# Performance work log

Hardware: AMD Instinct MI355X
Metric: run time of the kernel (lower is better)

The kernel has to match this reference:

```python
import jax, jax.numpy as jnp
import numpy as np

B, N, C, H = 2, 2048, 512, 8
D = C // H
SCALE = D ** (-0.5)


def setup_inputs() -> dict:
    key = jax.random.key(0)
    k1, k2, k3 = jax.random.split(key, 3)
    x = jax.random.normal(k1, (B, N, C), dtype=jnp.float32)
    qkv_w = jax.random.normal(k2, (C, 3 * C), dtype=jnp.float32) * (C ** -0.5)
    proj_w = jax.random.normal(k3, (C, C), dtype=jnp.float32) * (C ** -0.5)
    proj_b = jnp.zeros((C,), dtype=jnp.float32)
    return {"x": x, "qkv_w": qkv_w, "proj_w": proj_w, "proj_b": proj_b}


def reference(x, qkv_w, proj_w, proj_b):
    # qkv projection (no bias) -> (B, N, 3, H, D) -> (3, B, H, N, D)
    qkv = jnp.einsum('bnc,cf->bnf', x, qkv_w)
    qkv = qkv.reshape(B, N, 3, H, D).transpose(2, 0, 3, 1, 4)
    q, k, v = qkv[0], qkv[1], qkv[2]
    q = q * SCALE
    attn = jnp.einsum('bhid,bhjd->bhij', q, k)          # (B, H, N, N)
    attn = jax.nn.softmax(attn, axis=-1)
    out = jnp.einsum('bhij,bhjd->bhid', attn, v)         # (B, H, N, D)
    # Faithful to source: reshape (B,H,N,D) -> (B,N,C) WITHOUT transposing
    out = out.reshape(B, N, C)
    out = jnp.einsum('bnc,cd->bnd', out, proj_w) + proj_b
    return out
```

## Files before the change

### kernel.cpp

```cpp
#include <hip/hip_runtime.h>
#include <math.h>

constexpr int Bb = 2;
constexpr int Nn = 2048;
constexpr int Cc = 512;
constexpr int Hh = 8;
constexpr int Dd = 64;

typedef short short8 __attribute__((ext_vector_type(8)));
typedef float floatx4 __attribute__((ext_vector_type(4)));
typedef float floatx16 __attribute__((ext_vector_type(16)));

__device__ inline short8 bcs8(uint4 u) { return __builtin_bit_cast(short8, u); }

__device__ inline floatx4 mfma16(short8 a, short8 b, floatx4 c) {
    return __builtin_amdgcn_mfma_f32_16x16x32_bf16(a, b, c, 0, 0, 0);
}
__device__ inline floatx16 mfma32(short8 a, short8 b, floatx16 c) {
    return __builtin_amdgcn_mfma_f32_32x32x16_bf16(a, b, c, 0, 0, 0);
}

typedef __attribute__((address_space(1))) void gvoid;
typedef __attribute__((address_space(3))) void svoid;
__device__ inline void glds16(const void* g, void* l) {
    __builtin_amdgcn_global_load_lds((const gvoid*)g, (svoid*)l, 16, 0, 0);
}

#if __has_builtin(__builtin_amdgcn_exp2f)
#define EXP2(x) __builtin_amdgcn_exp2f(x)
#else
#define EXP2(x) __expf((x) * 0.69314718056f)
#endif

__device__ inline unsigned pk_trunc(float a, float b) {
    return __builtin_amdgcn_perm(__float_as_uint(b), __float_as_uint(a), 0x07060302u);
}
__device__ inline unsigned pk_rne(float a, float b) {
    unsigned ua = __float_as_uint(a); ua += 0x7fffu + ((ua >> 16) & 1u);
    unsigned ub = __float_as_uint(b); ub += 0x7fffu + ((ub >> 16) & 1u);
    return __builtin_amdgcn_perm(ub, ua, 0x07060302u);
}
__device__ inline unsigned short rne1(float a) {
    unsigned u = __float_as_uint(a); u += 0x7fffu + ((u >> 16) & 1u);
    return (unsigned short)(u >> 16);
}
__device__ inline float tr16(float a) {
    return __uint_as_float(__float_as_uint(a) & 0xffff0000u);
}
__device__ inline void split8(float4 A, float4 B, uint4& hi, uint4& lo) {
    hi = make_uint4(pk_trunc(A.x, A.y), pk_trunc(A.z, A.w),
                    pk_trunc(B.x, B.y), pk_trunc(B.z, B.w));
    lo = make_uint4(pk_trunc(A.x - tr16(A.x), A.y - tr16(A.y)),
                    pk_trunc(A.z - tr16(A.z), A.w - tr16(A.w)),
                    pk_trunc(B.x - tr16(B.x), B.y - tr16(B.y)),
                    pk_trunc(B.z - tr16(B.z), B.w - tr16(B.w)));
}

__global__ __launch_bounds__(256) void prep(const float* __restrict__ qkv_w,
                                            const float* __restrict__ proj_w,
                                            const float* __restrict__ x,
                                            unsigned short* __restrict__ wqh,
                                            unsigned short* __restrict__ wql,
                                            unsigned short* __restrict__ wph,
                                            unsigned short* __restrict__ wpl,
                                            unsigned short* __restrict__ xh,
                                            unsigned short* __restrict__ xl)
{
    __shared__ float Tl[64][68];
    int bid = blockIdx.x;
    if (bid >= 256) {
        size_t base = ((size_t)(bid - 256) * 256 + threadIdx.x) * 16;
        float4 a = *(const float4*)(x + base);
        float4 b = *(const float4*)(x + base + 4);
        float4 c = *(const float4*)(x + base + 8);
        float4 d = *(const float4*)(x + base + 12);
        uint4 h0, L0, h1, L1;
        split8(a, b, h0, L0); split8(c, d, h1, L1);
        *(uint4*)(xh + base) = h0; *(uint4*)(xh + base + 8) = h1;
        *(uint4*)(xl + base) = L0; *(uint4*)(xl + base + 8) = L1;
        return;
    }
    const float* src; unsigned short *dh, *dlo; int W, f0, k0;
    if (bid < 192) { int kt = bid / 24, ft = bid % 24; W = 1536; src = qkv_w; dh = wqh; dlo = wql; f0 = ft * 64; k0 = kt * 64; }
    else { int b2 = bid - 192; int kt = b2 / 8, ft = b2 % 8; W = 512; src = proj_w; dh = wph; dlo = wpl; f0 = ft * 64; k0 = kt * 64; }
    int t = threadIdx.x;
    {
        int kl = t >> 2, fc = (t & 3) * 16;
        const float* p = src + (size_t)(k0 + kl) * W + f0 + fc;
        #pragma unroll
        for (int i = 0; i < 4; ++i) {
            float4 v = *(const float4*)(p + i * 4);
            Tl[kl][fc + i * 4 + 0] = v.x; Tl[kl][fc + i * 4 + 1] = v.y;
            Tl[kl][fc + i * 4 + 2] = v.z; Tl[kl][fc + i * 4 + 3] = v.w;
        }
    }
    __syncthreads();
    {
        int fl = t >> 2, kc = (t & 3) * 16;
        float v[16];
        #pragma unroll
        for (int i = 0; i < 16; ++i) v[i] = Tl[kc + i][fl];
        unsigned hi[8], lo[8];
        #pragma unroll
        for (int i = 0; i < 8; ++i) {
            float a = v[2 * i], b = v[2 * i + 1];
            hi[i] = pk_trunc(a, b);
            lo[i] = pk_trunc(a - tr16(a), b - tr16(b));
        }
        unsigned short* oh = dh + (size_t)(f0 + fl) * 512 + k0 + kc;
        unsigned short* ol = dlo + (size_t)(f0 + fl) * 512 + k0 + kc;
        *(uint4*)oh = make_uint4(hi[0], hi[1], hi[2], hi[3]);
        *(uint4*)(oh + 8) = make_uint4(hi[4], hi[5], hi[6], hi[7]);
        *(uint4*)ol = make_uint4(lo[0], lo[1], lo[2], lo[3]);
        *(uint4*)(ol + 8) = make_uint4(lo[4], lo[5], lo[6], lo[7]);
    }
}

__global__ __launch_bounds__(256, 3) void gemm_qkv(const unsigned short* __restrict__ xh,
                                                   const unsigned short* __restrict__ xl,
                                                   const unsigned short* __restrict__ wh,
                                                   const unsigned short* __restrict__ wl,
                                                   unsigned short* __restrict__ qd,
                                                   unsigned short* __restrict__ kd,
                                                   unsigned short* __restrict__ vt)
{
    __shared__ __align__(16) char smem[49152];
    const int tid = threadIdx.x, lane = tid & 63, w = tid >> 6;
    const int l15 = lane & 15, l4 = lane >> 4;
    const int row0 = blockIdx.y * 128, col0 = blockIdx.x * 64;
    const int wm = w >> 1, wn = w & 1;

    floatx4 acc[4][2];
    #pragma unroll
    for (int i = 0; i < 4; ++i)
        #pragma unroll
        for (int j = 0; j < 2; ++j)
            #pragma unroll
            for (int r = 0; r < 4; ++r) acc[i][j][r] = 0.f;

    auto stage = [&](int k0, char* buf) {
        char* Ah = buf; char* Al = buf + 8192; char* Bh = buf + 16384; char* Bl = buf + 20480;
        #pragma unroll
        for (int i = 0; i < 4; ++i) {
            int sid = w * 4 + i; int mt = sid >> 1, comp = sid & 1;
            const unsigned short* src = (comp ? xl : xh) + (size_t)(row0 + mt * 16 + l15) * 512 + k0 + l4 * 8;
            glds16(src, (comp ? Al : Ah) + mt * 1024);
        }
        #pragma unroll
        for (int i = 0; i < 2; ++i) {
            int sid = w * 2 + i; int nt = sid >> 1, comp = sid & 1;
            const unsigned short* src = (comp ? wl : wh) + (size_t)(col0 + nt * 16 + l15) * 512 + k0 + l4 * 8;
            glds16(src, (comp ? Bl : Bh) + nt * 1024);
        }
    };

    stage(0, smem);
    for (int it = 0; it < 16; ++it) {
        __syncthreads();
        char* buf = smem + (it & 1) * 24576;
        if (it < 15) stage((it + 1) * 32, smem + ((it + 1) & 1) * 24576);
        char* Ah = buf; char* Al = buf + 8192; char* Bh = buf + 16384; char* Bl = buf + 20480;
        short8 af[4][2], bf[2][2];
        #pragma unroll
        for (int mt = 0; mt < 4; ++mt) {
            int off = ((wm * 4 + mt) << 10) + (lane << 4);
            af[mt][0] = bcs8(*(const uint4*)(Ah + off));
            af[mt][1] = bcs8(*(const uint4*)(Al + off));
        }
        #pragma unroll
        for (int nt = 0; nt < 2; ++nt) {
            int off = ((wn * 2 + nt) << 10) + (lane << 4);
            bf[nt][0] = bcs8(*(const uint4*)(Bh + off));
            bf[nt][1] = bcs8(*(const uint4*)(Bl + off));
        }
        #pragma unroll
        for (int mt = 0; mt < 4; ++mt)
            #pragma unroll
            for (int nt = 0; nt < 2; ++nt) {
                acc[mt][nt] = mfma16(af[mt][0], bf[nt][0], acc[mt][nt]);
                acc[mt][nt] = mfma16(af[mt][0], bf[nt][1], acc[mt][nt]);
                acc[mt][nt] = mfma16(af[mt][1], bf[nt][0], acc[mt][nt]);
            }
    }
    #pragma unroll
    for (int mt = 0; mt < 4; ++mt)
        #pragma unroll
        for (int nt = 0; nt < 2; ++nt) {
            int c = col0 + (wn * 2 + nt) * 16 + l15;
            int which = c >> 9;
            int head = (c >> 6) & 7, d = c & 63;
            int tokb = row0 + (wm * 4 + mt) * 16 + l4 * 4;
            int b = tokb >> 11, n = tokb & 2047;
            if (which == 2) {
                uint2 pv;
                pv.x = pk_rne(acc[mt][nt][0], acc[mt][nt][1]);
                pv.y = pk_rne(acc[mt][nt][2], acc[mt][nt][3]);
                *(uint2*)&vt[((size_t)((b * 8 + head) * 64 + d)) * 2048 + n] = pv;
            } else {
                unsigned short* dst = which ? kd : qd;
                float s = which ? 1.0f : 0.18033688f;
                #pragma unroll
                for (int r = 0; r < 4; ++r)
                    dst[(size_t)((b * 8 + head) * 2048 + n + r) * 64 + d] = rne1(acc[mt][nt][r] * s);
            }
        }
}

__global__ __launch_bounds__(512, 4) void attn(const unsigned short* __restrict__ qd,
                                               const unsigned short* __restrict__ kd,
                                               const unsigned short* __restrict__ vt,
                                               unsigned short* __restrict__ Oh,
                                               unsigned short* __restrict__ Ol)
{
    __shared__ __align__(16) char smem[65536];

    int bid = blockIdx.x;
    int xcd = bid & 7; int rr = bid >> 3;
    int qt = rr & 31; int bhi = rr >> 5;
    int bh = (bhi << 3) | xcd;
    int tid = threadIdx.x, lane = tid & 63, w = tid >> 6;
    int qg = w >> 2, kg = w & 3;
    int l31 = lane & 31, h = lane >> 5;

    short8 qf[4];
    #pragma unroll
    for (int s = 0; s < 4; ++s)
        qf[s] = bcs8(*(const uint4*)(qd + ((size_t)bh * 2048 + qt * 64 + qg * 32 + l31) * 64 + s * 16 + h * 8));

    const uint4 onesu = make_uint4(0x3F803F80u, 0x3F803F80u, 0x3F803F80u, 0x3F803F80u);
    const short8 onesf = bcs8(onesu);

    floatx16 OT[2], OTl;
    #pragma unroll
    for (int i = 0; i < 2; ++i)
        #pragma unroll
        for (int r = 0; r < 16; ++r) OT[i][r] = 0.f;
    #pragma unroll
    for (int r = 0; r < 16; ++r) OTl[r] = 0.f;

    auto stage = [&](int c, char* buf) {
        int ks0 = c * 128;
        #pragma unroll
        for (int i = 0; i < 4; ++i) {
            int sid = w * 4 + i;
            if (sid < 16) {
                int mt = sid >> 2, s = sid & 3;
                const unsigned short* src = kd + (size_t)(bh * 2048 + ks0 + mt * 32 + l31) * 64 + s * 16 + h * 8;
                glds16(src, buf + sid * 1024);
            } else {
                int s2 = sid - 16; int mtv = s2 >> 3, sv = s2 & 7;
                const unsigned short* src = vt + (size_t)(bh * 64 + mtv * 32 + l31) * 2048 + ks0 + sv * 16 + h * 8;
                glds16(src, buf + 16384 + s2 * 1024);
            }
        }
    };

    stage(0, smem);
    for (int c = 0; c < 16; ++c) {
        __syncthreads();
        char* cbuf = smem + (c & 1) * 32768;
        if (c < 15) stage(c + 1, smem + ((c + 1) & 1) * 32768);

        char* Kst = cbuf; char* Vst = cbuf + 16384;
        short8 kf[4];
        #pragma unroll
        for (int s = 0; s < 4; ++s)
            kf[s] = bcs8(*(const uint4*)(Kst + ((kg << 2) + s) * 1024 + (lane << 4)));
        short8 vf[2][2];
        #pragma unroll
        for (int kc = 0; kc < 2; ++kc) {
            int sv = kg * 2 + kc;
            vf[kc][0] = bcs8(*(const uint4*)(Vst + sv * 1024 + (lane << 4)));
            vf[kc][1] = bcs8(*(const uint4*)(Vst + (8 + sv) * 1024 + (lane << 4)));
        }

        floatx16 st;
        #pragma unroll
        for (int r = 0; r < 16; ++r) st[r] = 0.f;
        #pragma unroll
        for (int s = 0; s < 4; ++s) st = mfma32(kf[s], qf[s], st);

        unsigned P2[8];
        #pragma unroll
        for (int s2 = 0; s2 < 8; ++s2)
            P2[s2] = pk_trunc(EXP2(st[2 * s2]), EXP2(st[2 * s2 + 1]));

        #pragma unroll
        for (int kc = 0; kc < 2; ++kc) {
            unsigned X0 = P2[4 * kc + 0], X1 = P2[4 * kc + 1];
            unsigned Y0 = P2[4 * kc + 2], Y1 = P2[4 * kc + 3];
            unsigned Xo0 = __shfl_xor(X0, 32, 64), Xo1 = __shfl_xor(X1, 32, 64);
            unsigned Yo0 = __shfl_xor(Y0, 32, 64), Yo1 = __shfl_xor(Y1, 32, 64);
            uint4 fu;
            fu.x = h ? Yo0 : X0;
            fu.y = h ? Yo1 : X1;
            fu.z = h ? Y0 : Xo0;
            fu.w = h ? Y1 : Xo1;
            short8 pf = bcs8(fu);
            OT[0] = mfma32(vf[kc][0], pf, OT[0]);
            OT[1] = mfma32(vf[kc][1], pf, OT[1]);
            OTl = mfma32(onesf, pf, OTl);
        }
    }

    float* Mq = (float*)smem + qg * 2048;
    float* Lq = (float*)(smem + 32768) + qg * 64;
    float* Tq = (float*)(smem + 32768 + 512) + qg * 2176;

    __syncthreads();
    if (kg == 3) {
        #pragma unroll
        for (int mtv = 0; mtv < 2; ++mtv)
            #pragma unroll
            for (int r = 0; r < 16; ++r) {
                int d = mtv * 32 + (r & 3) + 8 * (r >> 2) + 4 * h;
                Mq[d * 32 + l31] = OT[mtv][r];
            }
        Lq[h * 32 + l31] = OTl[0];
    }
    __syncthreads();
    if (kg == 2) {
        #pragma unroll
        for (int mtv = 0; mtv < 2; ++mtv)
            #pragma unroll
            for (int r = 0; r < 16; ++r) {
                int d = mtv * 32 + (r & 3) + 8 * (r >> 2) + 4 * h;
                Mq[d * 32 + l31] += OT[mtv][r];
            }
        Lq[h * 32 + l31] += OTl[0];
    }
    __syncthreads();
    if (kg == 1) {
        #pragma unroll
        for (int mtv = 0; mtv < 2; ++mtv)
            #pragma unroll
            for (int r = 0; r < 16; ++r) {
                int d = mtv * 32 + (r & 3) + 8 * (r >> 2) + 4 * h;
                Mq[d * 32 + l31] += OT[mtv][r];
            }
        Lq[h * 32 + l31] += OTl[0];
    }
    __syncthreads();
    if (kg == 0) {
        #pragma unroll
        for (int mtv = 0; mtv < 2; ++mtv)
            #pragma unroll
            for (int r = 0; r < 16; ++r) {
                int d = mtv * 32 + (r & 3) + 8 * (r >> 2) + 4 * h;
                OT[mtv][r] += Mq[d * 32 + l31];
            }
        float inv = 1.f / (Lq[h * 32 + l31] + OTl[0]);
        #pragma unroll
        for (int mtv = 0; mtv < 2; ++mtv)
            #pragma unroll
            for (int r = 0; r < 16; ++r) {
                int d = mtv * 32 + (r & 3) + 8 * (r >> 2) + 4 * h;
                Tq[l31 * 68 + d] = OT[mtv][r] * inv;
            }
    }
    __syncthreads();
    {
        int q = tid >> 3, dc = (tid & 7) * 8;
        const float* T = (const float*)(smem + 32768 + 512) + (q >> 5) * 2176;
        int ql = q & 31;
        float vv[8];
        #pragma unroll
        for (int i = 0; i < 8; ++i) vv[i] = T[ql * 68 + dc + i];
        unsigned hi[4], lo[4];
        #pragma unroll
        for (int i = 0; i < 4; ++i) {
            float a = vv[2 * i], bb = vv[2 * i + 1];
            hi[i] = pk_trunc(a, bb);
            lo[i] = pk_trunc(a - tr16(a), bb - tr16(bb));
        }
        size_t bo = ((size_t)(bh * 2048 + qt * 64 + q)) * 64 + dc;
        *(uint4*)(Oh + bo) = make_uint4(hi[0], hi[1], hi[2], hi[3]);
        *(uint4*)(Ol + bo) = make_uint4(lo[0], lo[1], lo[2], lo[3]);
    }
}

__global__ __launch_bounds__(256, 2) void gemm_proj(const unsigned short* __restrict__ Ah_g,
                                                    const unsigned short* __restrict__ Al_g,
                                                    const unsigned short* __restrict__ wh,
                                                    const unsigned short* __restrict__ wl,
                                                    const float* __restrict__ bias,
                                                    float* __restrict__ out)
{
    __shared__ __align__(16) char smem[32768];
    const int tid = threadIdx.x, lane = tid & 63, w = tid >> 6;
    const int l15 = lane & 15, l4 = lane >> 4;
    const int row0 = blockIdx.y * 64, col0 = blockIdx.x * 64;
    const int wm = w >> 1, wn = w & 1;

    floatx4 acc[2][2];
    #pragma unroll
    for (int i = 0; i < 2; ++i)
        #pragma unroll
        for (int j = 0; j < 2; ++j)
            #pragma unroll
            for (int r = 0; r < 4; ++r) acc[i][j][r] = 0.f;

    auto stage = [&](int k0, char* buf) {
        #pragma unroll
        for (int i = 0; i < 4; ++i) {
            int sid = w * 4 + i;
            if (sid < 8) {
                int mt = sid >> 1, comp = sid & 1;
                const unsigned short* src = (comp ? Al_g : Ah_g) + (size_t)(row0 + mt * 16 + l15) * 512 + k0 + l4 * 8;
                glds16(src, buf + (comp ? 4096 : 0) + mt * 1024);
            } else {
                int s2 = sid - 8; int nt = s2 >> 1, comp = s2 & 1;
                const unsigned short* src = (comp ? wl : wh) + (size_t)(col0 + nt * 16 + l15) * 512 + k0 + l4 * 8;
                glds16(src, buf + (comp ? 12288 : 8192) + nt * 1024);
            }
        }
    };

    stage(0, smem);
    for (int it = 0; it < 16; ++it) {
        __syncthreads();
        char* buf = smem + (it & 1) * 16384;
        if (it < 15) stage((it + 1) * 32, smem + ((it + 1) & 1) * 16384);
        char* Ah = buf; char* Al = buf + 4096; char* Bh = buf + 8192; char* Bl = buf + 12288;
        short8 af[2][2], bf[2][2];
        #pragma unroll
        for (int mt = 0; mt < 2; ++mt) {
            int off = ((wm * 2 + mt) << 10) + (lane << 4);
            af[mt][0] = bcs8(*(const uint4*)(Ah + off));
            af[mt][1] = bcs8(*(const uint4*)(Al + off));
        }
        #pragma unroll
        for (int nt = 0; nt < 2; ++nt) {
            int off = ((wn * 2 + nt) << 10) + (lane << 4);
            bf[nt][0] = bcs8(*(const uint4*)(Bh + off));
            bf[nt][1] = bcs8(*(const uint4*)(Bl + off));
        }
        #pragma unroll
        for (int mt = 0; mt < 2; ++mt)
            #pragma unroll
            for (int nt = 0; nt < 2; ++nt) {
                acc[mt][nt] = mfma16(af[mt][0], bf[nt][0], acc[mt][nt]);
                acc[mt][nt] = mfma16(af[mt][0], bf[nt][1], acc[mt][nt]);
                acc[mt][nt] = mfma16(af[mt][1], bf[nt][0], acc[mt][nt]);
            }
    }
    #pragma unroll
    for (int mt = 0; mt < 2; ++mt)
        #pragma unroll
        for (int nt = 0; nt < 2; ++nt) {
            int c = col0 + (wn * 2 + nt) * 16 + l15;
            float bv = bias[c];
            #pragma unroll
            for (int r = 0; r < 4; ++r) {
                int tok = row0 + (wm * 2 + mt) * 16 + l4 * 4 + r;
                out[(size_t)tok * 512 + c] = acc[mt][nt][r] + bv;
            }
        }
}

extern "C" void kernel_launch(void* const* d_in, const int* in_sizes, int n_in,
                              void* d_out, int out_size, void* d_ws, size_t ws_size,
                              hipStream_t stream)
{
    const float* x      = (const float*)d_in[0];
    const float* qkv_w  = (const float*)d_in[1];
    const float* proj_w = (const float*)d_in[2];
    const float* proj_b = (const float*)d_in[3];
    float* out = (float*)d_out;

    char* ws = (char*)d_ws;
    unsigned short* qd   = (unsigned short*)ws;
    unsigned short* kd   = (unsigned short*)(ws + 4194304);
    unsigned short* vt   = (unsigned short*)(ws + 8388608);
    unsigned short* wqh  = (unsigned short*)(ws + 12582912);
    unsigned short* wql  = (unsigned short*)(ws + 14155776);
    unsigned short* wph  = (unsigned short*)(ws + 15728640);
    unsigned short* wpl  = (unsigned short*)(ws + 16252928);
    unsigned short* Oh   = (unsigned short*)(ws + 16777216);
    unsigned short* Ol   = (unsigned short*)(ws + 20971520);
    unsigned short* xh = Oh;
    unsigned short* xl = Ol;

    prep<<<768, 256, 0, stream>>>(qkv_w, proj_w, x, wqh, wql, wph, wpl, xh, xl);
    gemm_qkv<<<dim3(24, 32), 256, 0, stream>>>(xh, xl, wqh, wql, qd, kd, vt);
    attn<<<512, 512, 0, stream>>>(qd, kd, vt, Oh, Ol);
    gemm_proj<<<dim3(8, 64), 256, 0, stream>>>(Oh, Ol, wph, wpl, proj_b, out);
}
```

Baseline: 165.7 us.

## Fuse x bf16 split into QKV GEMM, load K to registers in attention

Removes the x hi/lo split pass from the prep kernel. The QKV GEMM now stages raw fp32 x tiles into LDS and splits them into bf16 hi/lo in registers just before the MFMAs, which avoids writing and re-reading two bf16 copies of x. In the attention kernel, K fragments are loaded straight from global memory into double-buffered registers instead of going through LDS, and LDS now stages only V, so shared memory shrinks. The P-fragment shuffle also drops from four cross-half shuffles to two per step, at the cost of more VGPRs and redundant per-block split arithmetic.

After: 173.2 us. 4.5% more time.

```diff
diff --git a/kernel.cpp b/kernel.cpp
--- a/kernel.cpp
+++ b/kernel.cpp
@@ -12,6 +12,7 @@
 typedef float floatx16 __attribute__((ext_vector_type(16)));
 
 __device__ inline short8 bcs8(uint4 u) { return __builtin_bit_cast(short8, u); }
+__device__ inline float4 bcf4(uint4 u) { return __builtin_bit_cast(float4, u); }
 
 __device__ inline floatx4 mfma16(short8 a, short8 b, floatx4 c) {
     return __builtin_amdgcn_mfma_f32_16x16x32_bf16(a, b, c, 0, 0, 0);
@@ -58,28 +59,13 @@
 
 __global__ __launch_bounds__(256) void prep(const float* __restrict__ qkv_w,
                                             const float* __restrict__ proj_w,
-                                            const float* __restrict__ x,
                                             unsigned short* __restrict__ wqh,
                                             unsigned short* __restrict__ wql,
                                             unsigned short* __restrict__ wph,
-                                            unsigned short* __restrict__ wpl,
-                                            unsigned short* __restrict__ xh,
-                                            unsigned short* __restrict__ xl)
+                                            unsigned short* __restrict__ wpl)
 {
     __shared__ float Tl[64][68];
     int bid = blockIdx.x;
-    if (bid >= 256) {
-        size_t base = ((size_t)(bid - 256) * 256 + threadIdx.x) * 16;
-        float4 a = *(const float4*)(x + base);
-        float4 b = *(const float4*)(x + base + 4);
-        float4 c = *(const float4*)(x + base + 8);
-        float4 d = *(const float4*)(x + base + 12);
-        uint4 h0, L0, h1, L1;
-        split8(a, b, h0, L0); split8(c, d, h1, L1);
-        *(uint4*)(xh + base) = h0; *(uint4*)(xh + base + 8) = h1;
-        *(uint4*)(xl + base) = L0; *(uint4*)(xl + base + 8) = L1;
-        return;
-    }
     const float* src; unsigned short *dh, *dlo; int W, f0, k0;
     if (bid < 192) { int kt = bid / 24, ft = bid % 24; W = 1536; src = qkv_w; dh = wqh; dlo = wql; f0 = ft * 64; k0 = kt * 64; }
     else { int b2 = bid - 192; int kt = b2 / 8, ft = b2 % 8; W = 512; src = proj_w; dh = wph; dlo = wpl; f0 = ft * 64; k0 = kt * 64; }
@@ -116,8 +102,7 @@
     }
 }
 
-__global__ __launch_bounds__(256, 3) void gemm_qkv(const unsigned short* __restrict__ xh,
-                                                   const unsigned short* __restrict__ xl,
+__global__ __launch_bounds__(256, 3) void gemm_qkv(const float* __restrict__ x,
                                                    const unsigned short* __restrict__ wh,
                                                    const unsigned short* __restrict__ wl,
                                                    unsigned short* __restrict__ qd,
@@ -139,18 +124,17 @@
             for (int r = 0; r < 4; ++r) acc[i][j][r] = 0.f;
 
     auto stage = [&](int k0, char* buf) {
-        char* Ah = buf; char* Al = buf + 8192; char* Bh = buf + 16384; char* Bl = buf + 20480;
         #pragma unroll
         for (int i = 0; i < 4; ++i) {
-            int sid = w * 4 + i; int mt = sid >> 1, comp = sid & 1;
-            const unsigned short* src = (comp ? xl : xh) + (size_t)(row0 + mt * 16 + l15) * 512 + k0 + l4 * 8;
-            glds16(src, (comp ? Al : Ah) + mt * 1024);
+            int sid = w * 4 + i; int mt = sid >> 1, sub = sid & 1;
+            const float* src = x + (size_t)(row0 + mt * 16 + l15) * 512 + k0 + l4 * 8 + sub * 4;
+            glds16(src, buf + sid * 1024);
         }
         #pragma unroll
         for (int i = 0; i < 2; ++i) {
             int sid = w * 2 + i; int nt = sid >> 1, comp = sid & 1;
             const unsigned short* src = (comp ? wl : wh) + (size_t)(col0 + nt * 16 + l15) * 512 + k0 + l4 * 8;
-            glds16(src, (comp ? Bl : Bh) + nt * 1024);
+            glds16(src, buf + 16384 + comp * 4096 + nt * 1024);
         }
     };
 
@@ -159,13 +143,17 @@
         __syncthreads();
         char* buf = smem + (it & 1) * 24576;
         if (it < 15) stage((it + 1) * 32, smem + ((it + 1) & 1) * 24576);
-        char* Ah = buf; char* Al = buf + 8192; char* Bh = buf + 16384; char* Bl = buf + 20480;
+        char* Ab = buf; char* Bh = buf + 16384; char* Bl = buf + 20480;
         short8 af[4][2], bf[2][2];
         #pragma unroll
         for (int mt = 0; mt < 4; ++mt) {
-            int off = ((wm * 4 + mt) << 10) + (lane << 4);
-            af[mt][0] = bcs8(*(const uint4*)(Ah + off));
-            af[mt][1] = bcs8(*(const uint4*)(Al + off));
+            int off = (((wm * 4 + mt) * 2) << 10) + (lane << 4);
+            float4 fa = bcf4(*(const uint4*)(Ab + off));
+            float4 fb = bcf4(*(const uint4*)(Ab + off + 1024));
+            uint4 hi, lo;
+            split8(fa, fb, hi, lo);
+            af[mt][0] = bcs8(hi);
+            af[mt][1] = bcs8(lo);
         }
         #pragma unroll
         for (int nt = 0; nt < 2; ++nt) {
@@ -212,7 +200,7 @@
                                                unsigned short* __restrict__ Oh,
                                                unsigned short* __restrict__ Ol)
 {
-    __shared__ __align__(16) char smem[65536];
+    __shared__ __align__(16) char smem[51200];
 
     int bid = blockIdx.x;
     int xcd = bid & 7; int rr = bid >> 3;
@@ -238,34 +226,34 @@
     #pragma unroll
     for (int r = 0; r < 16; ++r) OTl[r] = 0.f;
 
-    auto stage = [&](int c, char* buf) {
+    auto stageV = [&](int c, char* buf) {
         int ks0 = c * 128;
         #pragma unroll
-        for (int i = 0; i < 4; ++i) {
-            int sid = w * 4 + i;
-            if (sid < 16) {
-                int mt = sid >> 2, s = sid & 3;
-                const unsigned short* src = kd + (size_t)(bh * 2048 + ks0 + mt * 32 + l31) * 64 + s * 16 + h * 8;
-                glds16(src, buf + sid * 1024);
-            } else {
-                int s2 = sid - 16; int mtv = s2 >> 3, sv = s2 & 7;
-                const unsigned short* src = vt + (size_t)(bh * 64 + mtv * 32 + l31) * 2048 + ks0 + sv * 16 + h * 8;
-                glds16(src, buf + 16384 + s2 * 1024);
-            }
+        for (int i = 0; i < 2; ++i) {
+            int sid = w * 2 + i; int mtv = sid >> 3, sv = sid & 7;
+            const unsigned short* src = vt + (size_t)(bh * 64 + mtv * 32 + l31) * 2048 + ks0 + sv * 16 + h * 8;
+            glds16(src, buf + sid * 1024);
         }
     };
 
-    stage(0, smem);
+    const unsigned short* kb_ = kd + ((size_t)bh * 2048 + kg * 32 + l31) * 64 + h * 8;
+    uint4 kfb[2][4];
+    #pragma unroll
+    for (int s = 0; s < 4; ++s) kfb[0][s] = *(const uint4*)(kb_ + s * 16);
+    stageV(0, smem);
+
+    #pragma unroll
     for (int c = 0; c < 16; ++c) {
         __syncthreads();
-        char* cbuf = smem + (c & 1) * 32768;
-        if (c < 15) stage(c + 1, smem + ((c + 1) & 1) * 32768);
-
-        char* Kst = cbuf; char* Vst = cbuf + 16384;
-        short8 kf[4];
-        #pragma unroll
-        for (int s = 0; s < 4; ++s)
-            kf[s] = bcs8(*(const uint4*)(Kst + ((kg << 2) + s) * 1024 + (lane << 4)));
+        const int cur = c & 1;
+        char* Vst = smem + cur * 16384;
+        if (c < 15) {
+            stageV(c + 1, smem + (cur ^ 1) * 16384);
+            const unsigned short* kp = kb_ + (size_t)(c + 1) * 128 * 64;
+            #pragma unroll
+            for (int s = 0; s < 4; ++s) kfb[cur ^ 1][s] = *(const uint4*)(kp + s * 16);
+        }
+
         short8 vf[2][2];
         #pragma unroll
         for (int kc = 0; kc < 2; ++kc) {
@@ -278,7 +266,7 @@
         #pragma unroll
         for (int r = 0; r < 16; ++r) st[r] = 0.f;
         #pragma unroll
-        for (int s = 0; s < 4; ++s) st = mfma32(kf[s], qf[s], st);
+        for (int s = 0; s < 4; ++s) st = mfma32(bcs8(kfb[cur][s]), qf[s], st);
 
         unsigned P2[8];
         #pragma unroll
@@ -289,13 +277,15 @@
         for (int kc = 0; kc < 2; ++kc) {
             unsigned X0 = P2[4 * kc + 0], X1 = P2[4 * kc + 1];
             unsigned Y0 = P2[4 * kc + 2], Y1 = P2[4 * kc + 3];
-            unsigned Xo0 = __shfl_xor(X0, 32, 64), Xo1 = __shfl_xor(X1, 32, 64);
-            unsigned Yo0 = __shfl_xor(Y0, 32, 64), Yo1 = __shfl_xor(Y1, 32, 64);
+            unsigned T0 = h ? X0 : Y0;
+            unsigned T1 = h ? X1 : Y1;
+            unsigned To0 = __shfl_xor(T0, 32, 64);
+            unsigned To1 = __shfl_xor(T1, 32, 64);
             uint4 fu;
-            fu.x = h ? Yo0 : X0;
-            fu.y = h ? Yo1 : X1;
-            fu.z = h ? Y0 : Xo0;
-            fu.w = h ? Y1 : Xo1;
+            fu.x = h ? To0 : X0;
+            fu.y = h ? To1 : X1;
+            fu.z = h ? Y0 : To0;
+            fu.w = h ? Y1 : To1;
             short8 pf = bcs8(fu);
             OT[0] = mfma32(vf[kc][0], pf, OT[0]);
             OT[1] = mfma32(vf[kc][1], pf, OT[1]);
@@ -305,7 +295,7 @@
 
     float* Mq = (float*)smem + qg * 2048;
     float* Lq = (float*)(smem + 32768) + qg * 64;
-    float* Tq = (float*)(smem + 32768 + 512) + qg * 2176;
+    float* Tq = (float*)(smem + 33280) + qg * 2176;
 
     __syncthreads();
     if (kg == 3) {
@@ -361,7 +351,7 @@
     __syncthreads();
     {
         int q = tid >> 3, dc = (tid & 7) * 8;
-        const float* T = (const float*)(smem + 32768 + 512) + (q >> 5) * 2176;
+        const float* T = (const float*)(smem + 33280) + (q >> 5) * 2176;
         int ql = q & 31;
         float vv[8];
         #pragma unroll
@@ -478,11 +468,9 @@
     unsigned short* wpl  = (unsigned short*)(ws + 16252928);
     unsigned short* Oh   = (unsigned short*)(ws + 16777216);
     unsigned short* Ol   = (unsigned short*)(ws + 20971520);
-    unsigned short* xh = Oh;
-    unsigned short* xl = Ol;
-
-    prep<<<768, 256, 0, stream>>>(qkv_w, proj_w, x, wqh, wql, wph, wpl, xh, xl);
-    gemm_qkv<<<dim3(24, 32), 256, 0, stream>>>(xh, xl, wqh, wql, qd, kd, vt);
+
+    prep<<<256, 256, 0, stream>>>(qkv_w, proj_w, wqh, wql, wph, wpl);
+    gemm_qkv<<<dim3(24, 32), 256, 0, stream>>>(x, wqh, wql, qd, kd, vt);
     attn<<<512, 512, 0, stream>>>(qd, kd, vt, Oh, Ol);
     gemm_proj<<<dim3(8, 64), 256, 0, stream>>>(Oh, Ol, wph, wpl, proj_b, out);
 }
```
